# Kernel optimization log

Hardware: AMD Instinct MI355X
Metric: run time of the kernel (lower is better)

Reference implementation:

```python
import jax, jax.numpy as jnp
import numpy as np

N = 100000          # num_nodes
E = 1600000         # num_edges (avg degree 16)
FEAT = 16           # z-embedding dim
IN_DIM = FEAT + 4   # + 4 physics scalars
HID = 128           # hidden_dim
NUM_LAYERS = 2
NUM_REL = 3
NUM_TYPES = 4
LN_EPS = 1e-5


def setup_inputs() -> dict:
    key = jax.random.key(0)
    ks = jax.random.split(key, 20)
    s = 0.05
    return {
        "z": jax.random.randint(ks[0], (N,), 0, 100),
        "sd": jax.random.normal(ks[1], (N, 1), jnp.float32),
        "df": jax.random.normal(ks[2], (N, 1), jnp.float32),
        "cond": jax.random.normal(ks[3], (N, 1), jnp.float32),
        "mult": jax.random.normal(ks[4], (N, 1), jnp.float32),
        "node_type": jax.random.randint(ks[5], (N,), 0, NUM_TYPES),
        "edge_index": jax.random.randint(ks[6], (2, E), 0, N),
        "edge_type": jax.random.randint(ks[7], (E,), 0, NUM_REL),
        # parameters
        "z_embed": jax.random.normal(ks[8], (100, FEAT), jnp.float32) * s,
        "enc_W1": jax.random.normal(ks[9], (NUM_TYPES, IN_DIM, HID), jnp.float32) * s,
        "enc_b1": jnp.zeros((NUM_TYPES, HID), jnp.float32),
        "enc_W2": jax.random.normal(ks[10], (NUM_TYPES, HID, HID), jnp.float32) * s,
        "enc_b2": jnp.zeros((NUM_TYPES, HID), jnp.float32),
        "lin_W": jax.random.normal(ks[11], (NUM_LAYERS, HID, HID), jnp.float32) * s,
        "lin_b": jnp.zeros((NUM_LAYERS, HID), jnp.float32),
        "rel_W": jax.random.normal(ks[12], (NUM_LAYERS, NUM_REL, HID, HID), jnp.float32) * s,
        "ln_g": jnp.ones((NUM_LAYERS, HID), jnp.float32),
        "ln_b": jnp.zeros((NUM_LAYERS, HID), jnp.float32),
        "reg_W": jax.random.normal(ks[13], (HID, 1), jnp.float32) * s,
        "reg_b": jnp.zeros((1,), jnp.float32),
    }


def reference(z, sd, df, cond, mult, node_type, edge_index, edge_type,
              z_embed, enc_W1, enc_b1, enc_W2, enc_b2,
              lin_W, lin_b, rel_W, ln_g, ln_b, reg_W, reg_b):
    # FeatureBuilder: [z embedding | 4 physics scalars] -> [N, IN_DIM]
    raw = jnp.concatenate([z_embed[z], sd, df, cond, mult], axis=1)
    n = raw.shape[0]

    # TypeSpecificEncoder: per-node-type 2-layer MLP, selected by node_type
    x = jnp.zeros((n, enc_W2.shape[-1]), raw.dtype)
    for t in range(enc_W1.shape[0]):
        h = jax.nn.relu(raw @ enc_W1[t] + enc_b1[t]) @ enc_W2[t] + enc_b2[t]
        x = jnp.where((node_type == t)[:, None], h, x)

    src, dst = edge_index[0], edge_index[1]
    # degree over ALL edges (as in the torch code), clamped to >= 1
    deg = jax.ops.segment_sum(jnp.ones(src.shape[0], x.dtype), dst, num_segments=n)
    deg = jnp.clip(deg, 1.0)[:, None]

    # stacked MultiRelationGNNLayer: gather -> per-relation matmul -> scatter-add
    for l in range(lin_W.shape[0]):
        xs = x[src]                               # [E, HID] gather
        msg = jnp.zeros_like(xs)
        for r in range(rel_W.shape[1]):
            mask_r = (edge_type == r)[:, None].astype(x.dtype)
            msg = msg + (xs @ rel_W[l, r]) * mask_r
        agg = jax.ops.segment_sum(msg, dst, num_segments=n) / deg
        h = x @ lin_W[l] + lin_b[l] + agg
        # LayerNorm
        mu = jnp.mean(h, axis=-1, keepdims=True)
        var = jnp.mean((h - mu) ** 2, axis=-1, keepdims=True)
        x = (h - mu) / jnp.sqrt(var + LN_EPS) * ln_g[l] + ln_b[l]

    pooled = jnp.mean(x, axis=0)                  # [HID]
    return pooled @ reg_W + reg_b                 # [1]
```

## Files before the change

### kernel.cpp

```cpp
#include <hip/hip_runtime.h>

#define NN 100000
#define NE 1600000
#define HD 128
#define IND 20
#define LNEPS 1e-5f
#define NLIST2 400000
#define NBKT 3125
#define PASSA_B 256
#define EDGES_PER_B 6250
#define FILL_B 256
#define WCAT_B 512
#define WCATE_B 256
#define W1P_B 128
#define FILLN_B 400
#define ENC_B 12500
#define NWIN 2
#define WINB 1563
#define ASTRIDE 260
#define SORT_CAP 4096
#define PAD_PER_BKT 672
#define NEP (NE + NBKT * PAD_PER_BKT)
#define H1S 136
#define AES 72

typedef unsigned int uint32;
typedef unsigned short ushort16;
typedef __attribute__((ext_vector_type(8))) short bf16x8;
typedef __attribute__((ext_vector_type(4))) float f32x4;
typedef __attribute__((ext_vector_type(2))) float f32x2;

__device__ __forceinline__ ushort16 f2bf(float f) {
    uint32 u = __float_as_uint(f);
    u += 0x7fffu + ((u >> 16) & 1u);
    return (ushort16)(u >> 16);
}
__device__ __forceinline__ float bf2f1(ushort16 h) {
    return __uint_as_float(((uint32)h) << 16);
}
__device__ __forceinline__ uint32 pack2bf(float2 v) {
    return (uint32)f2bf(v.x) | ((uint32)f2bf(v.y) << 16);
}


__global__ __launch_bounds__(256) void k_hist(const int* __restrict__ ei,
                                              const int* __restrict__ et,
                                              int* __restrict__ H,
                                              ushort16* __restrict__ key16,
                                              unsigned* __restrict__ hdr32,
                                              const float* __restrict__ W2,
                                              ushort16* __restrict__ Weh,
                                              ushort16* __restrict__ Wel,
                                              const float* __restrict__ W1,
                                              ushort16* __restrict__ W1e,
                                              const int* __restrict__ nt,
                                              int* misc, unsigned* nodelist,
                                              uint32* x0, uint32* x1) {
    __shared__ int hist[NBKT];
    __shared__ int cnt4[4][4];
    __shared__ int base4[4];
    int bid = blockIdx.x, tid = threadIdx.x;

    if (bid >= PASSA_B + WCATE_B + W1P_B) {
        int rb = bid - PASSA_B - WCATE_B - W1P_B;
        int lane = tid & 63;
        int w = tid >> 6;
        if (rb == 0 && tid < 32) {
            x0[(size_t)NN * 32 + tid] = 0;
            x1[(size_t)NN * 32 + tid] = 0;
        }
        int i = rb * 256 + tid;
        int t = (i < NN) ? nt[i] : -1;
        unsigned long long lt = (lane == 63) ? ~0ull >> 1
                              : (((unsigned long long)1 << (lane + 1)) - 1) >> 1;
        lt = ((unsigned long long)1 << lane) - 1;
        int pre[4], wc[4];
#pragma unroll
        for (int tt = 0; tt < 4; tt++) {
            unsigned long long m = __ballot(t == tt);
            pre[tt] = (int)__popcll(m & lt);
            wc[tt] = (int)__popcll(m);
        }
        if (lane == 0) {
            cnt4[w][0] = wc[0]; cnt4[w][1] = wc[1];
            cnt4[w][2] = wc[2]; cnt4[w][3] = wc[3];
        }
        __syncthreads();
        if (tid < 4) {
            int tot = cnt4[0][tid] + cnt4[1][tid] + cnt4[2][tid] + cnt4[3][tid];
            base4[tid] = tot ? atomicAdd(&misc[8 + tid], tot) : 0;
        }
        __syncthreads();
        if (t >= 0) {
            int off = base4[t] + pre[t];
#pragma unroll
            for (int wp = 0; wp < 3; wp++) if (wp < w) off += cnt4[wp][t];
            nodelist[t * NN + off] = (unsigned)i | ((unsigned)t << 17);
        }
        return;
    }
    if (bid >= PASSA_B + WCATE_B) {
        int idx = (bid - PASSA_B - WCATE_B) * 256 + tid;
        int jj = idx & 7;
        int lane = (idx >> 3) & 63;
        int ntile = (idx >> 9) & 7;
        int kstep = (idx >> 12) & 1;
        int t = (idx >> 13) & 3;
        int ke = kstep * 32 + ((lane >> 4) * 8) + jj;
        int n = ntile * 16 + (lane & 15);
        float w = 0.f;
        int sel = 0;
        if (ke < 60) {
            int k0 = ke / 3;
            sel = ke - 3 * k0;
            w = W1[((size_t)t * IND + k0) * HD + n];
        }
        ushort16 hi = f2bf(w);
        W1e[idx] = (sel == 2) ? f2bf(w - bf2f1(hi)) : hi;
        return;
    }
    if (bid >= PASSA_B) {
        int idx = (bid - PASSA_B) * 256 + tid;
        int jj = idx & 7;
        int lane = (idx >> 3) & 63;
        int ntile = (idx >> 9) & 7;
        int kt = (idx >> 12) & 3;
        int t = (idx >> 14) & 3;
        int k = kt * 32 + ((lane >> 4) * 8) + jj;
        int n = ntile * 16 + (lane & 15);
        float v = W2[((size_t)t * HD + k) * HD + n];
        ushort16 hi = f2bf(v);
        Weh[idx] = hi;
        Wel[idx] = f2bf(v - bf2f1(hi));
        return;
    }

    for (int k = tid; k < NBKT; k += 256) hist[k] = 0;
    __syncthreads();
    int e0 = bid * EDGES_PER_B, e1 = e0 + EDGES_PER_B;
    for (int e = e0 + tid; e < e1; e += 256) {
        int d = ei[NE + e];
        int s = ei[e];
        int r = et[e];
        int bkt = d >> 5;
        key16[e] = (ushort16)bkt;
        hdr32[e] = (unsigned)s | ((unsigned)r << 17) | ((unsigned)(d & 31) << 19);
        atomicAdd(&hist[bkt], 1);
    }
    __syncthreads();
    for (int k = tid; k < NBKT; k += 256) H[bid * NBKT + k] = hist[k];
}


__global__ __launch_bounds__(256) void k_s1(int* __restrict__ H, int* __restrict__ btot) {
    int bkt = blockIdx.x * 256 + threadIdx.x;
    if (bkt >= NBKT) return;
    int run = 0;
    for (int jm = 0; jm < PASSA_B; jm += 8) {
        int t0 = H[(jm + 0) * NBKT + bkt];
        int t1 = H[(jm + 1) * NBKT + bkt];
        int t2 = H[(jm + 2) * NBKT + bkt];
        int t3 = H[(jm + 3) * NBKT + bkt];
        int t4 = H[(jm + 4) * NBKT + bkt];
        int t5 = H[(jm + 5) * NBKT + bkt];
        int t6 = H[(jm + 6) * NBKT + bkt];
        int t7 = H[(jm + 7) * NBKT + bkt];
        H[(jm + 0) * NBKT + bkt] = run; run += t0;
        H[(jm + 1) * NBKT + bkt] = run; run += t1;
        H[(jm + 2) * NBKT + bkt] = run; run += t2;
        H[(jm + 3) * NBKT + bkt] = run; run += t3;
        H[(jm + 4) * NBKT + bkt] = run; run += t4;
        H[(jm + 5) * NBKT + bkt] = run; run += t5;
        H[(jm + 6) * NBKT + bkt] = run; run += t6;
        H[(jm + 7) * NBKT + bkt] = run; run += t7;
    }
    btot[bkt] = run;
}

__global__ __launch_bounds__(1024) void k_s2(const int* __restrict__ btot,
                                             int* __restrict__ boff) {
    __shared__ int s[1024];
    int t = threadIdx.x;
    int v4[4];
    int sum = 0;
#pragma unroll
    for (int i = 0; i < 4; i++) {
        int idx = t * 4 + i;
        v4[i] = (idx < NBKT) ? btot[idx] : 0;
        sum += v4[i];
    }
    s[t] = sum;
    __syncthreads();
    for (int o = 1; o < 1024; o <<= 1) {
        int tv = (t >= o) ? s[t - o] : 0;
        __syncthreads();
        s[t] += tv;
        __syncthreads();
    }
    int run = s[t] - sum;
#pragma unroll
    for (int i = 0; i < 4; i++) {
        int idx = t * 4 + i;
        if (idx < NBKT) boff[idx] = run;
        run += v4[i];
    }
    if (t == 1023) boff[NBKT] = NE;
}


__global__ __launch_bounds__(256) void k_fill2(
        const ushort16* __restrict__ key16, const unsigned* __restrict__ hdr32,
        const int* __restrict__ H, const int* __restrict__ boff,
        unsigned* __restrict__ packed,
        const unsigned* __restrict__ nodelist, const int* __restrict__ z,
        const float* __restrict__ sd, const float* __restrict__ df,
        const float* __restrict__ cond, const float* __restrict__ mult,
        const float* __restrict__ z_embed,
        const ushort16* __restrict__ W1e, const float* __restrict__ b1,
        const float* __restrict__ b2,
        unsigned char* __restrict__ xout,
        const float* __restrict__ rel_W, const float* __restrict__ lin_W,
        ushort16* __restrict__ Wbh, ushort16* __restrict__ Wbl,
        const ushort16* __restrict__ Weh, const ushort16* __restrict__ Wel) {
    __shared__ __attribute__((aligned(16))) char smem[13440];
    int bid = blockIdx.x;
    int tid = threadIdx.x;

    if (bid < FILL_B) {
        int* cur = (int*)smem;
        int e0 = bid * EDGES_PER_B, e1 = e0 + EDGES_PER_B;
        for (int w = 0; w < NWIN; w++) {
            int lo = w * WINB;
            for (int k = tid; k < WINB; k += 256) {
                int bkt = lo + k;
                cur[k] = (bkt < NBKT) ? (boff[bkt] + H[bid * NBKT + bkt]) : 0;
            }
            __syncthreads();
            for (int e = e0 + tid; e < e1; e += 256) {
                int kb = (int)key16[e];
                unsigned d = (unsigned)(kb - lo);
                if (d < (unsigned)WINB) {
                    int p = atomicAdd(&cur[d], 1);
                    packed[p] = hdr32[e];
                }
            }
            __syncthreads();
        }
        return;
    }
    int j = bid - FILL_B;
    if (j < WCAT_B) {
        int idx = j * 256 + tid;
        int jj = idx & 7;
        int lane = (idx >> 3) & 63;
        int ntile = (idx >> 9) & 7;
        int kt = (idx >> 12) & 15;
        int l = (idx >> 16) & 1;
        int k = kt * 32 + ((lane >> 4) * 8) + jj;
        int n = ntile * 16 + (lane & 15);
        float v;
        if (k < 384) v = rel_W[((l * 3 + (k >> 7)) * HD + (k & 127)) * HD + n];
        else         v = lin_W[(l * HD + (k - 384)) * HD + n];
        ushort16 hi = f2bf(v);
        Wbh[idx] = hi;
        Wbl[idx] = f2bf(v - bf2f1(hi));
        return;
    }
    j -= WCAT_B;
    if (j >= ENC_B) return;

    ushort16* Ae  = (ushort16*)smem;
    ushort16* h1b = (ushort16*)(smem + 4608);
    unsigned* ent = (unsigned*)(smem + 4608 + 8704);

    int base = j * 32;
    if (tid < 32) ent[tid] = nodelist[base + tid];
    if (tid >= 64 && tid < 128) {
        int r = (tid - 64) >> 1, c = 30 + (tid & 1);
        ((uint32*)Ae)[r * 36 + c] = 0;
    }
    __syncthreads();
    if (ent[0] == 0xFFFFFFFFu) return;
    int type = (int)(ent[0] >> 17);

    for (int idx = tid; idx < 32 * 20; idx += 256) {
        int nl = idx / 20, f = idx - nl * 20;
        unsigned e = ent[nl];
        float v = 0.f;
        if (e != 0xFFFFFFFFu) {
            int node = (int)(e & 0x1FFFF);
            if (f < 16)      v = z_embed[z[node] * 16 + f];
            else if (f == 16) v = sd[node];
            else if (f == 17) v = df[node];
            else if (f == 18) v = cond[node];
            else              v = mult[node];
        }
        ushort16 hi = f2bf(v);
        ushort16 lo = f2bf(v - bf2f1(hi));
        ushort16* ap = Ae + nl * AES + 3 * f;
        ap[0] = hi; ap[1] = lo; ap[2] = hi;
    }
    __syncthreads();

    int lane = tid & 63, wv = tid >> 6;
    int nt0 = 2 * wv, nt1 = 2 * wv + 1;
    int mrow0 = lane & 15, mrow1 = 16 + (lane & 15);
    int koff = (lane >> 4) * 8;

    {
        f32x4 e00 = {0.f, 0.f, 0.f, 0.f}, e01 = e00, e10 = e00, e11 = e00;
        const bf16x8* w1p = (const bf16x8*)(W1e + (size_t)type * 8192);
#pragma unroll
        for (int ks = 0; ks < 2; ks++) {
            bf16x8 af0 = *(const bf16x8*)&Ae[mrow0 * AES + ks * 32 + koff];
            bf16x8 af1 = *(const bf16x8*)&Ae[mrow1 * AES + ks * 32 + koff];
            bf16x8 bf0 = w1p[(ks * 8 + nt0) * 64 + lane];
            bf16x8 bf1 = w1p[(ks * 8 + nt1) * 64 + lane];
            e00 = __builtin_amdgcn_mfma_f32_16x16x32_bf16(af0, bf0, e00, 0, 0, 0);
            e01 = __builtin_amdgcn_mfma_f32_16x16x32_bf16(af0, bf1, e01, 0, 0, 0);
            e10 = __builtin_amdgcn_mfma_f32_16x16x32_bf16(af1, bf0, e10, 0, 0, 0);
            e11 = __builtin_amdgcn_mfma_f32_16x16x32_bf16(af1, bf1, e11, 0, 0, 0);
        }
        int c0 = nt0 * 16 + (lane & 15), c1 = nt1 * 16 + (lane & 15);
        float bb0 = b1[type * HD + c0], bb1 = b1[type * HD + c1];
        int rb2 = (lane >> 4) * 4;
#pragma unroll
        for (int r = 0; r < 4; r++) {
            h1b[(rb2 + r) * H1S + c0]      = f2bf(fmaxf(e00[r] + bb0, 0.f));
            h1b[(rb2 + r) * H1S + c1]      = f2bf(fmaxf(e01[r] + bb1, 0.f));
            h1b[(16 + rb2 + r) * H1S + c0] = f2bf(fmaxf(e10[r] + bb0, 0.f));
            h1b[(16 + rb2 + r) * H1S + c1] = f2bf(fmaxf(e11[r] + bb1, 0.f));
        }
    }
    __syncthreads();

    f32x4 a00 = {0.f, 0.f, 0.f, 0.f}, a01 = a00, a10 = a00, a11 = a00;
    const bf16x8* weh = (const bf16x8*)(Weh + (size_t)type * 16384);
    const bf16x8* wel = (const bf16x8*)(Wel + (size_t)type * 16384);
    const ushort16* h1p = h1b;
#pragma unroll
    for (int kt = 0; kt < 4; kt++) {
        bf16x8 af0 = *(const bf16x8*)&h1p[mrow0 * H1S + kt * 32 + koff];
        bf16x8 af1 = *(const bf16x8*)&h1p[mrow1 * H1S + kt * 32 + koff];
        bf16x8 bh0 = weh[(kt * 8 + nt0) * 64 + lane];
        bf16x8 bh1 = weh[(kt * 8 + nt1) * 64 + lane];
        bf16x8 bl0 = wel[(kt * 8 + nt0) * 64 + lane];
        bf16x8 bl1 = wel[(kt * 8 + nt1) * 64 + lane];
        a00 = __builtin_amdgcn_mfma_f32_16x16x32_bf16(af0, bh0, a00, 0, 0, 0);
        a01 = __builtin_amdgcn_mfma_f32_16x16x32_bf16(af0, bh1, a01, 0, 0, 0);
        a10 = __builtin_amdgcn_mfma_f32_16x16x32_bf16(af1, bh0, a10, 0, 0, 0);
        a11 = __builtin_amdgcn_mfma_f32_16x16x32_bf16(af1, bh1, a11, 0, 0, 0);
        a00 = __builtin_amdgcn_mfma_f32_16x16x32_bf16(af0, bl0, a00, 0, 0, 0);
        a01 = __builtin_amdgcn_mfma_f32_16x16x32_bf16(af0, bl1, a01, 0, 0, 0);
        a10 = __builtin_amdgcn_mfma_f32_16x16x32_bf16(af1, bl0, a10, 0, 0, 0);
        a11 = __builtin_amdgcn_mfma_f32_16x16x32_bf16(af1, bl1, a11, 0, 0, 0);
    }
    int c0 = nt0 * 16 + (lane & 15), c1 = nt1 * 16 + (lane & 15);
    float b20 = b2[type * HD + c0], b21 = b2[type * HD + c1];
    int rb = (lane >> 4) * 4;
#pragma unroll
    for (int r = 0; r < 4; r++) {
        int r0 = rb + r, r1 = 16 + rb + r;
        unsigned e0v = ent[r0], e1v = ent[r1];
        if (e0v != 0xFFFFFFFFu) {
            int node = (int)(e0v & 0x1FFFF);
            int p0 = __builtin_amdgcn_cvt_pk_fp8_f32(a00[r] + b20, a00[r] + b20, 0, false);
            int p1 = __builtin_amdgcn_cvt_pk_fp8_f32(a01[r] + b21, a01[r] + b21, 0, false);
            xout[(size_t)node * HD + c0] = (unsigned char)(p0 & 0xff);
            xout[(size_t)node * HD + c1] = (unsigned char)(p1 & 0xff);
        }
        if (e1v != 0xFFFFFFFFu) {
            int node = (int)(e1v & 0x1FFFF);
            int p0 = __builtin_amdgcn_cvt_pk_fp8_f32(a10[r] + b20, a10[r] + b20, 0, false);
            int p1 = __builtin_amdgcn_cvt_pk_fp8_f32(a11[r] + b21, a11[r] + b21, 0, false);
            xout[(size_t)node * HD + c0] = (unsigned char)(p0 & 0xff);
            xout[(size_t)node * HD + c1] = (unsigned char)(p1 & 0xff);
        }
    }
}


__global__ __launch_bounds__(256) void k_sort2(const unsigned* __restrict__ packed,
                                               const int* __restrict__ boff,
                                               unsigned* __restrict__ packed2,
                                               int* __restrict__ off,
                                               int* __restrict__ degarr) {
    __shared__ unsigned ebuf[SORT_CAP];
    __shared__ int hs[96];
    __shared__ int cur[96];
    __shared__ int segp[97];
    int b = blockIdx.x;
    int tid = threadIdx.x;
    int base = boff[b];
    int tot = boff[b + 1] - base;
    if (tot > SORT_CAP) tot = SORT_CAP;
    int pb = base + PAD_PER_BKT * b;

    if (tid < 96) hs[tid] = 0;
    for (int e = tid; e < tot; e += 256) ebuf[e] = packed[base + e];
    __syncthreads();
    for (int e = tid; e < tot; e += 256) {
        unsigned h = ebuf[e];
        int key = (int)(h >> 19) * 3 + (int)((h >> 17) & 3);
        atomicAdd(&hs[key], 1);
    }
    __syncthreads();
    if (tid == 0) {
        int run = 0;
        for (int k = 0; k < 96; k++) {
            segp[k] = run;
            run += (hs[k] + 7) & ~7;
        }
        segp[96] = run;
    }
    __syncthreads();
    if (tid < 96) {
        cur[tid] = segp[tid];
        off[((b * 32 + tid / 3) << 2) + (tid % 3)] = pb + segp[tid];
    }
    if (tid >= 96 && tid < 128) {
        int n = tid - 96;
        off[((b * 32 + n) << 2) + 3] = pb + segp[3 * n + 3];
        degarr[b * 32 + n] = hs[3 * n] + hs[3 * n + 1] + hs[3 * n + 2];
    }
    __syncthreads();
    for (int e = tid; e < tot; e += 256) {
        unsigned h = ebuf[e];
        int key = (int)(h >> 19) * 3 + (int)((h >> 17) & 3);
        int p = atomicAdd(&cur[key], 1);
        packed2[pb + p] = h & 0x1FFFF;
    }
    __syncthreads();
    if (tid < 96) {
        int e0 = segp[tid] + hs[tid];
        int e1 = segp[tid + 1];
        for (int q = e0; q < e1; q++) packed2[pb + q] = NN;
    }
}


#define LOADU8(U, Q)                                                          \
    U##0 = x[(int)Q##0 * 64 + lane]; U##1 = x[(int)Q##1 * 64 + lane];         \
    U##2 = x[(int)Q##2 * 64 + lane]; U##3 = x[(int)Q##3 * 64 + lane];         \
    U##4 = x[(int)Q##4 * 64 + lane]; U##5 = x[(int)Q##5 * 64 + lane];         \
    U##6 = x[(int)Q##6 * 64 + lane]; U##7 = x[(int)Q##7 * 64 + lane];

#define LOADQ8(Q, E)                                                          \
    Q##0 = packed[(E)];     Q##1 = packed[(E) + 1];                           \
    Q##2 = packed[(E) + 2]; Q##3 = packed[(E) + 3];                           \
    Q##4 = packed[(E) + 4]; Q##5 = packed[(E) + 5];                           \
    Q##6 = packed[(E) + 6]; Q##7 = packed[(E) + 7];

#define SUM8(S, U) {                                                          \
    f32x2 v0 = __builtin_amdgcn_cvt_pk_f32_fp8(U##0, false);                  \
    f32x2 v1 = __builtin_amdgcn_cvt_pk_f32_fp8(U##1, false);                  \
    f32x2 v2 = __builtin_amdgcn_cvt_pk_f32_fp8(U##2, false);                  \
    f32x2 v3 = __builtin_amdgcn_cvt_pk_f32_fp8(U##3, false);                  \
    f32x2 v4 = __builtin_amdgcn_cvt_pk_f32_fp8(U##4, false);                  \
    f32x2 v5 = __builtin_amdgcn_cvt_pk_f32_fp8(U##5, false);                  \
    f32x2 v6 = __builtin_amdgcn_cvt_pk_f32_fp8(U##6, false);                  \
    f32x2 v7 = __builtin_amdgcn_cvt_pk_f32_fp8(U##7, false);                  \
    S = ((v0 + v1) + (v2 + v3)) + ((v4 + v5) + (v6 + v7)); }

__global__ __launch_bounds__(512, 6) void k_fused(
        const ushort16* __restrict__ x,
        const unsigned* __restrict__ packed,
        const int* __restrict__ off, const int* __restrict__ degarr,
        const ushort16* __restrict__ Wbh, const ushort16* __restrict__ Wbl,
        const float* __restrict__ lb, const float* __restrict__ g,
        const float* __restrict__ bta, unsigned char* __restrict__ xout,
        const float* __restrict__ regW, float* __restrict__ partials) {
    __shared__ uint32 Alds[32 * ASTRIDE];
    __shared__ float stat[32][2];
    __shared__ float red[8];
    int tid = threadIdx.x;
    int lane = tid & 63;
    int wv = tid >> 6;
    int nb = blockIdx.x * 32;

    int bv = off[((nb + wv * 4) << 2) + lane];
    int dgv = degarr[nb + wv * 4 + (lane & 3)];

#pragma unroll
    for (int p = 0; p < 2; p++) {
        int nodeA = nb + wv * 4 + 2 * p;
        int nodeB = nodeA + 1;
        int bA0 = __builtin_amdgcn_readlane(bv, 8 * p + 0);
        int bA1 = __builtin_amdgcn_readlane(bv, 8 * p + 1);
        int bA2 = __builtin_amdgcn_readlane(bv, 8 * p + 2);
        int bA3 = __builtin_amdgcn_readlane(bv, 8 * p + 3);
        int bB0 = __builtin_amdgcn_readlane(bv, 8 * p + 4);
        int bB1 = __builtin_amdgcn_readlane(bv, 8 * p + 5);
        int bB2 = __builtin_amdgcn_readlane(bv, 8 * p + 6);
        int bB3 = __builtin_amdgcn_readlane(bv, 8 * p + 7);
        int dgA = __builtin_amdgcn_readlane(dgv, 2 * p);
        int dgB = __builtin_amdgcn_readlane(dgv, 2 * p + 1);
        float idA = 1.0f / (float)(dgA > 0 ? dgA : 1);
        float idB = 1.0f / (float)(dgB > 0 ? dgB : 1);
        int usA = x[nodeA * 64 + lane];
        int usB = x[nodeB * 64 + lane];
        f32x2 aA0 = {0.f, 0.f}, aA1 = aA0, aA2 = aA0;
        f32x2 aB0 = aA0, aB1 = aA0, aB2 = aA0;
        int eA = bA0, eB = bB0;
        unsigned qA0, qA1, qA2, qA3, qA4, qA5, qA6, qA7;
        unsigned qB0, qB1, qB2, qB3, qB4, qB5, qB6, qB7;
        if (eA < bA3) { LOADQ8(qA, eA) }
        if (eB < bB3) { LOADQ8(qB, eB) }
        while (true) {
            bool dA = eA < bA3, dB = eB < bB3;
            if (!dA && !dB) break;
            int uA0, uA1, uA2, uA3, uA4, uA5, uA6, uA7;
            int uB0, uB1, uB2, uB3, uB4, uB5, uB6, uB7;
            if (dA) { LOADU8(uA, qA) }
            if (dB) { LOADU8(uB, qB) }
            if (dA) { LOADQ8(qA, eA + 8) }
            if (dB) { LOADQ8(qB, eB + 8) }
            if (dA) {
                f32x2 s; SUM8(s, uA)
                if (eA < bA1)      aA0 += s;
                else if (eA < bA2) aA1 += s;
                else               aA2 += s;
                eA += 8;
            }
            if (dB) {
                f32x2 s; SUM8(s, uB)
                if (eB < bB1)      aB0 += s;
                else if (eB < bB2) aB1 += s;
                else               aB2 += s;
                eB += 8;
            }
        }
        uint32* arA = Alds + (wv * 4 + 2 * p) * ASTRIDE;
        uint32* arB = arA + ASTRIDE;
        f32x2 vsA = __builtin_amdgcn_cvt_pk_f32_fp8(usA, false);
        f32x2 vsB = __builtin_amdgcn_cvt_pk_f32_fp8(usB, false);
        arA[lane]       = pack2bf(make_float2(aA0.x * idA, aA0.y * idA));
        arA[64 + lane]  = pack2bf(make_float2(aA1.x * idA, aA1.y * idA));
        arA[128 + lane] = pack2bf(make_float2(aA2.x * idA, aA2.y * idA));
        arA[192 + lane] = pack2bf(make_float2(vsA.x, vsA.y));
        arB[lane]       = pack2bf(make_float2(aB0.x * idB, aB0.y * idB));
        arB[64 + lane]  = pack2bf(make_float2(aB1.x * idB, aB1.y * idB));
        arB[128 + lane] = pack2bf(make_float2(aB2.x * idB, aB2.y * idB));
        arB[192 + lane] = pack2bf(make_float2(vsB.x, vsB.y));
    }
    __syncthreads();

    f32x4 acc00 = {0.f, 0.f, 0.f, 0.f}, acc10 = acc00;
    int mrow0 = (lane & 15);
    int mrow1 = 16 + (lane & 15);
    int q4 = (lane >> 4) * 4;
    const bf16x8* wbh = (const bf16x8*)Wbh;
    const bf16x8* wbl = (const bf16x8*)Wbl;

#pragma unroll 4
    for (int kt = 0; kt < 16; kt++) {
        bf16x8 af0 = *(const bf16x8*)&Alds[mrow0 * ASTRIDE + kt * 16 + q4];
        bf16x8 af1 = *(const bf16x8*)&Alds[mrow1 * ASTRIDE + kt * 16 + q4];
        bf16x8 bh0 = wbh[(kt * 8 + wv) * 64 + lane];
        bf16x8 bl0 = wbl[(kt * 8 + wv) * 64 + lane];
        acc00 = __builtin_amdgcn_mfma_f32_16x16x32_bf16(af0, bh0, acc00, 0, 0, 0);
        acc10 = __builtin_amdgcn_mfma_f32_16x16x32_bf16(af1, bh0, acc10, 0, 0, 0);
        acc00 = __builtin_amdgcn_mfma_f32_16x16x32_bf16(af0, bl0, acc00, 0, 0, 0);
        acc10 = __builtin_amdgcn_mfma_f32_16x16x32_bf16(af1, bl0, acc10, 0, 0, 0);
    }
    __syncthreads();

    float* hlds = (float*)Alds;
    int n0 = wv * 16 + (lane & 15);
    float bj0 = lb[n0];
    int rbase = (lane >> 4) * 4;
#pragma unroll
    for (int r = 0; r < 4; r++) {
        hlds[(rbase + r) * 132 + n0]      = acc00[r] + bj0;
        hlds[(16 + rbase + r) * 132 + n0] = acc10[r] + bj0;
    }
    __syncthreads();

    {
        int node = tid >> 4, l16 = tid & 15;
        float s = 0.f, ss = 0.f;
#pragma unroll
        for (int i = 0; i < 8; i++) {
            float v = hlds[node * 132 + l16 + 16 * i];
            s += v; ss += v * v;
        }
        for (int d = 8; d >= 1; d >>= 1) {
            s += __shfl_down(s, d, 16);
            ss += __shfl_down(ss, d, 16);
        }
        if (l16 == 0) {
            float mu = s * (1.f / 128.f);
            float var = ss * (1.f / 128.f) - mu * mu;
            stat[node][0] = mu;
            stat[node][1] = rsqrtf(var + LNEPS);
        }
    }
    __syncthreads();

    {
        int node = tid >> 4, q16 = tid & 15;
        float mu = stat[node][0], rs = stat[node][1];
        const float* hr = hlds + node * 132 + q16 * 8;
        float vv[8];
#pragma unroll
        for (int k = 0; k < 8; k++) {
            int f = q16 * 8 + k;
            vv[k] = (hr[k] - mu) * rs * g[f] + bta[f];
        }
        if (regW == nullptr) {
            int w[2];
#pragma unroll
            for (int p = 0; p < 2; p++) {
                int pk = __builtin_amdgcn_cvt_pk_fp8_f32(vv[p * 4 + 0], vv[p * 4 + 1], 0, false);
                pk = __builtin_amdgcn_cvt_pk_fp8_f32(vv[p * 4 + 2], vv[p * 4 + 3], pk, true);
                w[p] = pk;
            }
            *(int2*)(xout + (size_t)(nb + node) * 128 + q16 * 8) = make_int2(w[0], w[1]);
        } else {
            float s = 0.f;
#pragma unroll
            for (int k = 0; k < 8; k++) s += vv[k] * regW[q16 * 8 + k];
            for (int d = 32; d >= 1; d >>= 1) s += __shfl_down(s, d);
            if (lane == 0) red[wv] = s;
            __syncthreads();
            if (tid == 0) {
                partials[blockIdx.x] = red[0] + red[1] + red[2] + red[3] +
                                       red[4] + red[5] + red[6] + red[7];
            }
        }
    }
}


__global__ __launch_bounds__(1024) void k_red(const float* __restrict__ partials,
                                              const float* __restrict__ reg_b,
                                              float* __restrict__ out) {
    __shared__ float s[16];
    int tid = threadIdx.x;
    float v = 0.f;
    for (int i = tid; i < NBKT; i += 1024) v += partials[i];
    for (int d = 32; d >= 1; d >>= 1) v += __shfl_down(v, d);
    if ((tid & 63) == 0) s[tid >> 6] = v;
    __syncthreads();
    if (tid == 0) {
        float t = 0.f;
#pragma unroll
        for (int i = 0; i < 16; i++) t += s[i];
        out[0] = t * (1.0f / (float)NN) + reg_b[0];
    }
}


extern "C" void kernel_launch(void* const* d_in, const int* in_sizes, int n_in,
                              void* d_out, int out_size, void* d_ws, size_t ws_size,
                              hipStream_t stream) {
    const int*   z       = (const int*)d_in[0];
    const float* sd      = (const float*)d_in[1];
    const float* df      = (const float*)d_in[2];
    const float* cond    = (const float*)d_in[3];
    const float* mult    = (const float*)d_in[4];
    const int*   nt      = (const int*)d_in[5];
    const int*   ei      = (const int*)d_in[6];
    const int*   et      = (const int*)d_in[7];
    const float* z_embed = (const float*)d_in[8];
    const float* enc_W1  = (const float*)d_in[9];
    const float* enc_b1  = (const float*)d_in[10];
    const float* enc_W2  = (const float*)d_in[11];
    const float* enc_b2  = (const float*)d_in[12];
    const float* lin_W   = (const float*)d_in[13];
    const float* lin_b   = (const float*)d_in[14];
    const float* rel_W   = (const float*)d_in[15];
    const float* ln_g    = (const float*)d_in[16];
    const float* ln_b    = (const float*)d_in[17];
    const float* reg_W   = (const float*)d_in[18];
    const float* reg_b   = (const float*)d_in[19];
    float* out = (float*)d_out;

    char* p = (char*)d_ws;
    int* H          = (int*)p;      p += (size_t)PASSA_B * NBKT * 4;
    int* btot       = (int*)p;      p += (size_t)4096 * 4;
    int* boff       = (int*)p;      p += (size_t)4096 * 4;
    int* misc       = (int*)p;      p += 16 * 4;
    float* partials = (float*)p;    p += (size_t)4096 * 4;
    int* off        = (int*)p;      p += (size_t)400384 * 4;
    int* degarr     = (int*)p;      p += (size_t)100096 * 4;
    ushort16* key16 = (ushort16*)p; p += (size_t)NE * 2;
    unsigned* hdr32 = (unsigned*)p; p += (size_t)NE * 4;
    unsigned* packed   = (unsigned*)p; p += (size_t)NE * 4;
    unsigned* packed2  = (unsigned*)p; p += (size_t)(NEP + 16) * 4;
    unsigned* nodelist = (unsigned*)p; p += (size_t)NLIST2 * 4;
    ushort16* Wbh   = (ushort16*)p; p += (size_t)2 * 512 * 128 * 2;
    ushort16* Wbl   = (ushort16*)p; p += (size_t)2 * 512 * 128 * 2;
    ushort16* Weh   = (ushort16*)p; p += (size_t)65536 * 2;
    ushort16* Wel   = (ushort16*)p; p += (size_t)65536 * 2;
    ushort16* W1e   = (ushort16*)p; p += (size_t)32768 * 2;
    unsigned char* x0 = (unsigned char*)p; p += (size_t)(NN + 1) * HD;
    unsigned char* x1 = (unsigned char*)p; p += (size_t)(NN + 1) * HD;

    hipMemsetAsync(misc, 0, 64, stream);
    hipMemsetAsync(nodelist, 0xFF, (size_t)NLIST2 * 4, stream);

    k_hist<<<PASSA_B + WCATE_B + W1P_B + FILLN_B, 256, 0, stream>>>(
        ei, et, H, key16, hdr32, enc_W2, Weh, Wel, enc_W1, W1e,
        nt, misc, nodelist, (uint32*)x0, (uint32*)x1);
    k_s1<<<13, 256, 0, stream>>>(H, btot);
    k_s2<<<1, 1024, 0, stream>>>(btot, boff);
    k_fill2<<<FILL_B + WCAT_B + ENC_B, 256, 0, stream>>>(
        key16, hdr32, H, boff, packed,
        nodelist, z, sd, df, cond, mult, z_embed,
        W1e, enc_b1, enc_b2, x0,
        rel_W, lin_W, Wbh, Wbl, Weh, Wel);
    k_sort2<<<NBKT, 256, 0, stream>>>(packed, boff, packed2, off, degarr);

    k_fused<<<NBKT, 512, 0, stream>>>((const ushort16*)x0, packed2, off, degarr,
                                      Wbh, Wbl,
                                      lin_b, ln_g, ln_b,
                                      x1, nullptr, partials);
    k_fused<<<NBKT, 512, 0, stream>>>((const ushort16*)x1, packed2, off, degarr,
                                      Wbh + (size_t)512 * 128, Wbl + (size_t)512 * 128,
                                      lin_b + HD, ln_g + HD, ln_b + HD,
                                      x0, reg_W, partials);
    k_red<<<1, 1024, 0, stream>>>(partials, reg_b, out);
}
```

Baseline: 350.2 us.

## Replace bucket sort with direct per-(node,relation) counting sort via global atomics

Replaces the two-level bucket histogram, scans, windowed fill and per-bucket local sort with a direct counting sort. It counts edges per (dst,relation) segment with global atomics, scans the padded segment sizes into offsets, and scatters src indices straight into the final padded CSR layout. This drops the intermediate key/header arrays, one kernel pass and the in-shared-memory sort. In exchange it relies on heavily contended global atomics and serialised per-thread padding loops, and order within a segment becomes nondeterministic.

```diff
diff --git a/kernel.cpp b/kernel.cpp
--- a/kernel.cpp
+++ b/kernel.cpp
@@ -7,20 +7,16 @@
 #define LNEPS 1e-5f
 #define NLIST2 400000
 #define NBKT 3125
-#define PASSA_B 256
-#define EDGES_PER_B 6250
-#define FILL_B 256
+#define PRE_B 512
+#define SCAT_B 1024
 #define WCAT_B 512
 #define WCATE_B 256
 #define W1P_B 128
 #define FILLN_B 400
 #define ENC_B 12500
-#define NWIN 2
-#define WINB 1563
+#define NSEG (3 * NN)
 #define ASTRIDE 260
-#define SORT_CAP 4096
-#define PAD_PER_BKT 672
-#define NEP (NE + NBKT * PAD_PER_BKT)
+#define NEP (NE + NSEG * 7)
 #define H1S 136
 #define AES 72
 
@@ -43,26 +39,23 @@
 }
 
 
-__global__ __launch_bounds__(256) void k_hist(const int* __restrict__ ei,
-                                              const int* __restrict__ et,
-                                              int* __restrict__ H,
-                                              ushort16* __restrict__ key16,
-                                              unsigned* __restrict__ hdr32,
-                                              const float* __restrict__ W2,
-                                              ushort16* __restrict__ Weh,
-                                              ushort16* __restrict__ Wel,
-                                              const float* __restrict__ W1,
-                                              ushort16* __restrict__ W1e,
-                                              const int* __restrict__ nt,
-                                              int* misc, unsigned* nodelist,
-                                              uint32* x0, uint32* x1) {
-    __shared__ int hist[NBKT];
+__global__ __launch_bounds__(256) void k_pre(const int* __restrict__ ei,
+                                             const int* __restrict__ et,
+                                             int* __restrict__ segcnt,
+                                             const float* __restrict__ W2,
+                                             ushort16* __restrict__ Weh,
+                                             ushort16* __restrict__ Wel,
+                                             const float* __restrict__ W1,
+                                             ushort16* __restrict__ W1e,
+                                             const int* __restrict__ nt,
+                                             int* misc, unsigned* nodelist,
+                                             uint32* x0, uint32* x1) {
     __shared__ int cnt4[4][4];
     __shared__ int base4[4];
     int bid = blockIdx.x, tid = threadIdx.x;
 
-    if (bid >= PASSA_B + WCATE_B + W1P_B) {
-        int rb = bid - PASSA_B - WCATE_B - W1P_B;
+    if (bid >= PRE_B + WCATE_B + W1P_B) {
+        int rb = bid - PRE_B - WCATE_B - W1P_B;
         int lane = tid & 63;
         int w = tid >> 6;
         if (rb == 0 && tid < 32) {
@@ -71,9 +64,7 @@
         }
         int i = rb * 256 + tid;
         int t = (i < NN) ? nt[i] : -1;
-        unsigned long long lt = (lane == 63) ? ~0ull >> 1
-                              : (((unsigned long long)1 << (lane + 1)) - 1) >> 1;
-        lt = ((unsigned long long)1 << lane) - 1;
+        unsigned long long lt = ((unsigned long long)1 << lane) - 1;
         int pre[4], wc[4];
 #pragma unroll
         for (int tt = 0; tt < 4; tt++) {
@@ -99,8 +90,8 @@
         }
         return;
     }
-    if (bid >= PASSA_B + WCATE_B) {
-        int idx = (bid - PASSA_B - WCATE_B) * 256 + tid;
+    if (bid >= PRE_B + WCATE_B) {
+        int idx = (bid - PRE_B - WCATE_B) * 256 + tid;
         int jj = idx & 7;
         int lane = (idx >> 3) & 63;
         int ntile = (idx >> 9) & 7;
@@ -119,8 +110,8 @@
         W1e[idx] = (sel == 2) ? f2bf(w - bf2f1(hi)) : hi;
         return;
     }
-    if (bid >= PASSA_B) {
-        int idx = (bid - PASSA_B) * 256 + tid;
+    if (bid >= PRE_B) {
+        int idx = (bid - PRE_B) * 256 + tid;
         int jj = idx & 7;
         int lane = (idx >> 3) & 63;
         int ntile = (idx >> 9) & 7;
@@ -135,83 +126,82 @@
         return;
     }
 
-    for (int k = tid; k < NBKT; k += 256) hist[k] = 0;
-    __syncthreads();
-    int e0 = bid * EDGES_PER_B, e1 = e0 + EDGES_PER_B;
+    int e0 = bid * (NE / PRE_B), e1 = e0 + (NE / PRE_B);
     for (int e = e0 + tid; e < e1; e += 256) {
         int d = ei[NE + e];
-        int s = ei[e];
         int r = et[e];
-        int bkt = d >> 5;
-        key16[e] = (ushort16)bkt;
-        hdr32[e] = (unsigned)s | ((unsigned)r << 17) | ((unsigned)(d & 31) << 19);
-        atomicAdd(&hist[bkt], 1);
-    }
-    __syncthreads();
-    for (int k = tid; k < NBKT; k += 256) H[bid * NBKT + k] = hist[k];
-}
-
-
-__global__ __launch_bounds__(256) void k_s1(int* __restrict__ H, int* __restrict__ btot) {
-    int bkt = blockIdx.x * 256 + threadIdx.x;
-    if (bkt >= NBKT) return;
-    int run = 0;
-    for (int jm = 0; jm < PASSA_B; jm += 8) {
-        int t0 = H[(jm + 0) * NBKT + bkt];
-        int t1 = H[(jm + 1) * NBKT + bkt];
-        int t2 = H[(jm + 2) * NBKT + bkt];
-        int t3 = H[(jm + 3) * NBKT + bkt];
-        int t4 = H[(jm + 4) * NBKT + bkt];
-        int t5 = H[(jm + 5) * NBKT + bkt];
-        int t6 = H[(jm + 6) * NBKT + bkt];
-        int t7 = H[(jm + 7) * NBKT + bkt];
-        H[(jm + 0) * NBKT + bkt] = run; run += t0;
-        H[(jm + 1) * NBKT + bkt] = run; run += t1;
-        H[(jm + 2) * NBKT + bkt] = run; run += t2;
-        H[(jm + 3) * NBKT + bkt] = run; run += t3;
-        H[(jm + 4) * NBKT + bkt] = run; run += t4;
-        H[(jm + 5) * NBKT + bkt] = run; run += t5;
-        H[(jm + 6) * NBKT + bkt] = run; run += t6;
-        H[(jm + 7) * NBKT + bkt] = run; run += t7;
-    }
-    btot[bkt] = run;
-}
-
-__global__ __launch_bounds__(1024) void k_s2(const int* __restrict__ btot,
-                                             int* __restrict__ boff) {
-    __shared__ int s[1024];
+        atomicAdd(&segcnt[d * 3 + r], 1);
+    }
+}
+
+
+__global__ __launch_bounds__(256) void k_scn1(const int* __restrict__ segcnt,
+                                              int* __restrict__ bsum) {
+    __shared__ int ws[4];
     int t = threadIdx.x;
-    int v4[4];
-    int sum = 0;
-#pragma unroll
-    for (int i = 0; i < 4; i++) {
-        int idx = t * 4 + i;
-        v4[i] = (idx < NBKT) ? btot[idx] : 0;
-        sum += v4[i];
-    }
-    s[t] = sum;
-    __syncthreads();
-    for (int o = 1; o < 1024; o <<= 1) {
-        int tv = (t >= o) ? s[t - o] : 0;
+    int n = blockIdx.x * 256 + t;
+    int tot = 0;
+    if (n < NN) {
+        int s0 = segcnt[3 * n], s1 = segcnt[3 * n + 1], s2 = segcnt[3 * n + 2];
+        tot = ((s0 + 7) & ~7) + ((s1 + 7) & ~7) + ((s2 + 7) & ~7);
+    }
+    int v = tot;
+    for (int d = 32; d >= 1; d >>= 1) v += __shfl_down(v, d);
+    if ((t & 63) == 0) ws[t >> 6] = v;
+    __syncthreads();
+    if (t == 0) bsum[blockIdx.x] = ws[0] + ws[1] + ws[2] + ws[3];
+}
+
+
+__global__ __launch_bounds__(256) void k_scn3(const int* __restrict__ segcnt,
+                                              const int* __restrict__ bsum,
+                                              int* __restrict__ off,
+                                              int* __restrict__ degarr,
+                                              int* __restrict__ cur,
+                                              unsigned* __restrict__ packed2) {
+    __shared__ int ls[256];
+    __shared__ int ws[4];
+    int b = blockIdx.x, t = threadIdx.x;
+    int part = 0;
+    for (int j = t; j < b; j += 256) part += bsum[j];
+    for (int d = 32; d >= 1; d >>= 1) part += __shfl_down(part, d);
+    if ((t & 63) == 0) ws[t >> 6] = part;
+    int n = b * 256 + t;
+    int s0 = 0, s1 = 0, s2 = 0;
+    if (n < NN) {
+        s0 = segcnt[3 * n]; s1 = segcnt[3 * n + 1]; s2 = segcnt[3 * n + 2];
+    }
+    int p80 = (s0 + 7) & ~7, p81 = (s1 + 7) & ~7, p82 = (s2 + 7) & ~7;
+    int tot = p80 + p81 + p82;
+    ls[t] = tot;
+    __syncthreads();
+    int gbase = ws[0] + ws[1] + ws[2] + ws[3];
+    for (int o = 1; o < 256; o <<= 1) {
+        int tv = (t >= o) ? ls[t - o] : 0;
         __syncthreads();
-        s[t] += tv;
+        ls[t] += tv;
         __syncthreads();
     }
-    int run = s[t] - sum;
-#pragma unroll
-    for (int i = 0; i < 4; i++) {
-        int idx = t * 4 + i;
-        if (idx < NBKT) boff[idx] = run;
-        run += v4[i];
-    }
-    if (t == 1023) boff[NBKT] = NE;
+    int base = gbase + ls[t] - tot;
+    if (n < NN) {
+        off[4 * n]     = base;
+        off[4 * n + 1] = base + p80;
+        off[4 * n + 2] = base + p80 + p81;
+        off[4 * n + 3] = base + tot;
+        degarr[n] = s0 + s1 + s2;
+        cur[3 * n]     = base;
+        cur[3 * n + 1] = base + p80;
+        cur[3 * n + 2] = base + p80 + p81;
+        for (int q = base + s0; q < base + p80; q++) packed2[q] = NN;
+        for (int q = base + p80 + s1; q < base + p80 + p81; q++) packed2[q] = NN;
+        for (int q = base + p80 + p81 + s2; q < base + tot; q++) packed2[q] = NN;
+    }
 }
 
 
 __global__ __launch_bounds__(256) void k_fill2(
-        const ushort16* __restrict__ key16, const unsigned* __restrict__ hdr32,
-        const int* __restrict__ H, const int* __restrict__ boff,
-        unsigned* __restrict__ packed,
+        const int* __restrict__ ei, const int* __restrict__ et,
+        int* __restrict__ cur, unsigned* __restrict__ packed2,
         const unsigned* __restrict__ nodelist, const int* __restrict__ z,
         const float* __restrict__ sd, const float* __restrict__ df,
         const float* __restrict__ cond, const float* __restrict__ mult,
@@ -226,29 +216,18 @@
     int bid = blockIdx.x;
     int tid = threadIdx.x;
 
-    if (bid < FILL_B) {
-        int* cur = (int*)smem;
-        int e0 = bid * EDGES_PER_B, e1 = e0 + EDGES_PER_B;
-        for (int w = 0; w < NWIN; w++) {
-            int lo = w * WINB;
-            for (int k = tid; k < WINB; k += 256) {
-                int bkt = lo + k;
-                cur[k] = (bkt < NBKT) ? (boff[bkt] + H[bid * NBKT + bkt]) : 0;
-            }
-            __syncthreads();
-            for (int e = e0 + tid; e < e1; e += 256) {
-                int kb = (int)key16[e];
-                unsigned d = (unsigned)(kb - lo);
-                if (d < (unsigned)WINB) {
-                    int p = atomicAdd(&cur[d], 1);
-                    packed[p] = hdr32[e];
-                }
-            }
-            __syncthreads();
+    if (bid < SCAT_B) {
+        int idx = bid * 256 + tid;
+        for (int e = idx; e < NE; e += SCAT_B * 256) {
+            int s = ei[e];
+            int d = ei[NE + e];
+            int r = et[e];
+            int p = atomicAdd(&cur[d * 3 + r], 1);
+            packed2[p] = (unsigned)s;
         }
         return;
     }
-    int j = bid - FILL_B;
+    int j = bid - SCAT_B;
     if (j < WCAT_B) {
         int idx = j * 256 + tid;
         int jj = idx & 7;
@@ -376,65 +355,6 @@
             xout[(size_t)node * HD + c0] = (unsigned char)(p0 & 0xff);
             xout[(size_t)node * HD + c1] = (unsigned char)(p1 & 0xff);
         }
-    }
-}
-
-
-__global__ __launch_bounds__(256) void k_sort2(const unsigned* __restrict__ packed,
-                                               const int* __restrict__ boff,
-                                               unsigned* __restrict__ packed2,
-                                               int* __restrict__ off,
-                                               int* __restrict__ degarr) {
-    __shared__ unsigned ebuf[SORT_CAP];
-    __shared__ int hs[96];
-    __shared__ int cur[96];
-    __shared__ int segp[97];
-    int b = blockIdx.x;
-    int tid = threadIdx.x;
-    int base = boff[b];
-    int tot = boff[b + 1] - base;
-    if (tot > SORT_CAP) tot = SORT_CAP;
-    int pb = base + PAD_PER_BKT * b;
-
-    if (tid < 96) hs[tid] = 0;
-    for (int e = tid; e < tot; e += 256) ebuf[e] = packed[base + e];
-    __syncthreads();
-    for (int e = tid; e < tot; e += 256) {
-        unsigned h = ebuf[e];
-        int key = (int)(h >> 19) * 3 + (int)((h >> 17) & 3);
-        atomicAdd(&hs[key], 1);
-    }
-    __syncthreads();
-    if (tid == 0) {
-        int run = 0;
-        for (int k = 0; k < 96; k++) {
-            segp[k] = run;
-            run += (hs[k] + 7) & ~7;
-        }
-        segp[96] = run;
-    }
-    __syncthreads();
-    if (tid < 96) {
-        cur[tid] = segp[tid];
-        off[((b * 32 + tid / 3) << 2) + (tid % 3)] = pb + segp[tid];
-    }
-    if (tid >= 96 && tid < 128) {
-        int n = tid - 96;
-        off[((b * 32 + n) << 2) + 3] = pb + segp[3 * n + 3];
-        degarr[b * 32 + n] = hs[3 * n] + hs[3 * n + 1] + hs[3 * n + 2];
-    }
-    __syncthreads();
-    for (int e = tid; e < tot; e += 256) {
-        unsigned h = ebuf[e];
-        int key = (int)(h >> 19) * 3 + (int)((h >> 17) & 3);
-        int p = atomicAdd(&cur[key], 1);
-        packed2[pb + p] = h & 0x1FFFF;
-    }
-    __syncthreads();
-    if (tid < 96) {
-        int e0 = segp[tid] + hs[tid];
-        int e1 = segp[tid + 1];
-        for (int q = e0; q < e1; q++) packed2[pb + q] = NN;
     }
 }
 
@@ -677,16 +597,13 @@
     float* out = (float*)d_out;
 
     char* p = (char*)d_ws;
-    int* H          = (int*)p;      p += (size_t)PASSA_B * NBKT * 4;
-    int* btot       = (int*)p;      p += (size_t)4096 * 4;
-    int* boff       = (int*)p;      p += (size_t)4096 * 4;
     int* misc       = (int*)p;      p += 16 * 4;
     float* partials = (float*)p;    p += (size_t)4096 * 4;
     int* off        = (int*)p;      p += (size_t)400384 * 4;
     int* degarr     = (int*)p;      p += (size_t)100096 * 4;
-    ushort16* key16 = (ushort16*)p; p += (size_t)NE * 2;
-    unsigned* hdr32 = (unsigned*)p; p += (size_t)NE * 4;
-    unsigned* packed   = (unsigned*)p; p += (size_t)NE * 4;
+    int* segcnt     = (int*)p;      p += (size_t)300032 * 4;
+    int* cur        = (int*)p;      p += (size_t)300032 * 4;
+    int* bsum       = (int*)p;      p += (size_t)512 * 4;
     unsigned* packed2  = (unsigned*)p; p += (size_t)(NEP + 16) * 4;
     unsigned* nodelist = (unsigned*)p; p += (size_t)NLIST2 * 4;
     ushort16* Wbh   = (ushort16*)p; p += (size_t)2 * 512 * 128 * 2;
@@ -698,19 +615,19 @@
     unsigned char* x1 = (unsigned char*)p; p += (size_t)(NN + 1) * HD;
 
     hipMemsetAsync(misc, 0, 64, stream);
+    hipMemsetAsync(segcnt, 0, (size_t)NSEG * 4, stream);
     hipMemsetAsync(nodelist, 0xFF, (size_t)NLIST2 * 4, stream);
 
-    k_hist<<<PASSA_B + WCATE_B + W1P_B + FILLN_B, 256, 0, stream>>>(
-        ei, et, H, key16, hdr32, enc_W2, Weh, Wel, enc_W1, W1e,
+    k_pre<<<PRE_B + WCATE_B + W1P_B + FILLN_B, 256, 0, stream>>>(
+        ei, et, segcnt, enc_W2, Weh, Wel, enc_W1, W1e,
         nt, misc, nodelist, (uint32*)x0, (uint32*)x1);
-    k_s1<<<13, 256, 0, stream>>>(H, btot);
-    k_s2<<<1, 1024, 0, stream>>>(btot, boff);
-    k_fill2<<<FILL_B + WCAT_B + ENC_B, 256, 0, stream>>>(
-        key16, hdr32, H, boff, packed,
+    k_scn1<<<(NN + 255) / 256, 256, 0, stream>>>(segcnt, bsum);
+    k_scn3<<<(NN + 255) / 256, 256, 0, stream>>>(segcnt, bsum, off, degarr, cur, packed2);
+    k_fill2<<<SCAT_B + WCAT_B + ENC_B, 256, 0, stream>>>(
+        ei, et, cur, packed2,
         nodelist, z, sd, df, cond, mult, z_embed,
         W1e, enc_b1, enc_b2, x0,
         rel_W, lin_W, Wbh, Wbl, Weh, Wel);
-    k_sort2<<<NBKT, 256, 0, stream>>>(packed, boff, packed2, off, degarr);
 
     k_fused<<<NBKT, 512, 0, stream>>>((const ushort16*)x0, packed2, off, degarr,
                                       Wbh, Wbl,
```

Result: slower. 479.6 us (+36.9%).
